# Optimization experiments

Hardware: AMD Instinct MI355X
Metric: run time of the kernel (lower is better)

Reference implementation:

```python
import jax, jax.numpy as jnp
import numpy as np

N, T, D, H = 100000, 16, 8, 40
HP1 = H + 1
ALPHA_DP = 1.0
KAPPA0 = 1000.0   # priorGaussianVarKappa
NU0 = 100.0       # priorWishartNu
PSI0_SCALE = 500.0  # priorWishartPsi = 500*I


def setup_inputs() -> dict:
    key = jax.random.key(0)
    ks = jax.random.split(key, 6)
    return {
        "BetaGamma1": jnp.ones((1, T), jnp.float32),
        "Phi": jax.random.uniform(ks[0], (N, T), jnp.float32),
        "inputData": jax.random.normal(ks[1], (N, D), jnp.float32),
        "outputData": jax.random.normal(ks[2], (N, 1), jnp.float32),
        "weightELM": jax.random.uniform(ks[3], (D, H), jnp.float32) * 2.0 - 1.0,
        "biasELM": jax.random.normal(ks[4], (H, 1), jnp.float32),
        "epsilonA": jnp.ones((1, T), jnp.float32),
        "epsilonB": jnp.ones((1, T), jnp.float32),
        "zetaA": 1e-4 * jnp.ones((1, T), jnp.float32),
        "zetaB": jnp.ones((1, T), jnp.float32),
    }


def reference(BetaGamma1, Phi, inputData, outputData, weightELM, biasELM,
              epsilonA, epsilonB, zetaA, zetaB):
    f32 = jnp.float32
    mu0 = jnp.zeros((D, 1), f32)                      # priorGaussianMeanMu
    Psi0 = PSI0_SCALE * jnp.eye(D, dtype=f32)         # priorWishartPsi

    sumPhi = jnp.sum(Phi, axis=0, keepdims=True)      # [1,T]

    # stick-breaking Beta params. Torch builds a flipped [T,N,T] tril mask;
    # mathematically BetaGamma2[t] = alpha + sum_{j>t} sum_n Phi[n,j]
    BetaGamma1_new = jnp.ones_like(BetaGamma1) + sumPhi
    col = sumPhi[0]                                   # [T]
    rev_incl = jnp.cumsum(col[::-1])[::-1]            # sum_{j>=t}
    BetaGamma2 = (ALPHA_DP + (rev_incl - col))[None, :]

    # Gaussian-Wishart natural-parameter updates.
    # Torch loops over clusters doing [N,D,D] bmm outer products; this is
    # S[:,:,t] = sum_n Phi[n,t] x_n x_n^T
    S = jnp.einsum('nt,ni,nj->ijt', Phi, inputData, inputData)  # [D,D,T]
    t11 = -0.5 * (Psi0 + KAPPA0 * mu0 @ mu0.T)[:, :, None] - 0.5 * S
    t12 = KAPPA0 * mu0 + inputData.T @ Phi            # [D,T]
    t21 = -0.5 * sumPhi - 0.5 * (NU0 + D + 2)         # [1,T]
    kappa = KAPPA0 + sumPhi                           # [1,T]
    mu = t12 / kappa                                  # [D,T]
    nu = -2.0 * t21 - 2.0 - float(D)                  # [1,T]
    psi = -2.0 * t11 - kappa[0][None, None, :] * jnp.einsum('it,jt->ijt', mu, mu)

    # ELM feature map + augmented design matrix X = [sigmoid(x W + b), 1]
    hmap = jax.nn.sigmoid(inputData @ weightELM + biasELM.T)   # [N,H]
    X = jnp.concatenate([hmap, jnp.ones((inputData.shape[0], 1), f32)], axis=1)  # [N,HP1]

    epsExp = (epsilonA / epsilonB)[0]                 # [T]
    zetaExp = (zetaA / zetaB)[0]                      # [T]

    # A[t] = X^T diag(Phi[:,t]) X   (torch: per-cluster bmm with diag_embed)
    A = jnp.einsum('nt,ni,nj->tij', Phi, X, X)        # [T,HP1,HP1]
    WS = jnp.linalg.inv(epsExp[:, None, None] * A
                        + zetaExp[:, None, None] * jnp.eye(HP1, dtype=f32))
    # b[t] = X^T diag(Phi[:,t]) y
    b = jnp.einsum('ni,nt->ti', X * outputData, Phi)  # [T,HP1]
    WMv = zetaExp[:, None] * jnp.einsum('tij,tj->ti', WS, b)   # [T,HP1]
    WM = WMv[:, :, None]                              # [T,HP1,1]

    # prior Zeta/Epsilon alias the variational initial values in __init__
    zetaA_new = zetaA + (H + 1) * 0.5
    zetaB_new = zetaB + 0.5 * (jnp.sum(WMv * WMv, axis=1)
                               + jnp.trace(WS, axis1=-2, axis2=-1))[None, :]
    epsA_new = epsilonA + 0.5 * sumPhi

    pred = jnp.einsum('ni,ti->tn', X, WMv)            # [T,N]
    err = outputData.T - pred                          # [T,N]
    t1 = jnp.einsum('tn,nt->t', err * err, Phi)[None, :]
    t2 = jnp.einsum('tij,tji->t', A, WS)[None, :]
    epsB_new = epsilonB + 0.5 * (t1 + t2)

    return (BetaGamma1_new, BetaGamma2, mu, kappa, nu, psi,
            WM, WS, zetaA_new, zetaB_new, epsA_new, epsB_new)
```

## Files before the change

kernel.cpp:

```cpp
#include <hip/hip_runtime.h>

#define Nn 100000
#define Tt 16
#define Dd 8
#define Hh 40
#define HP1 41

#define CSZ 53248
#define XEF_OFF  0
#define XEH_OFF  (XEF_OFF + 64 * Nn)
#define XEL_OFF  (XEH_OFF + 32 * Nn)
#define PHIT_OFF (XEL_OFF + 32 * Nn)
#define PART_OFF (PHIT_OFF + 16 * Nn)
#define P_OFF    (PART_OFF + 8 * CSZ)

#define OFF_BG1   0
#define OFF_BG2   16
#define OFF_MU    32
#define OFF_KAPPA 160
#define OFF_NU    176
#define OFF_PSI   192
#define OFF_WM    1216
#define OFF_WS    1872
#define OFF_ZA    28768
#define OFF_ZB    28784
#define OFF_EA    28800
#define OFF_EB    28816

typedef _Float16 f16x8 __attribute__((ext_vector_type(8)));
typedef float f32x4 __attribute__((ext_vector_type(4)));
typedef unsigned int u32x4 __attribute__((ext_vector_type(4)));

#define AIDX(i, t, j) ((((i) * 16 + (t)) * 64) + (j))

__global__ __launch_bounds__(256)
void elm_expand(const float* __restrict__ Phi, const float* __restrict__ Xd,
                const float* __restrict__ Yd, const float* __restrict__ W,
                const float* __restrict__ bb, float* __restrict__ XeF32,
                unsigned short* __restrict__ XeHi, unsigned short* __restrict__ XeLo,
                float* __restrict__ PhiT)
{
  __shared__ float sW[Dd * Hh];
  __shared__ float sb[Hh];
  __shared__ float xs[64][9];
  __shared__ float ys[64];
  __shared__ float hrow[64][41];
  __shared__ float pt[16][68];
  int tid = threadIdx.x;
  int n0 = blockIdx.x * 64;

  for (int i = tid; i < Dd * Hh; i += 256) sW[i] = W[i];
  if (tid < Hh) sb[tid] = bb[tid];
  if (tid < 128) {
    int nl = tid >> 1, h4 = (tid & 1) * 4;
    int gn = n0 + nl;
    float4 v = (gn < Nn) ? *(const float4*)(Xd + (size_t)gn * 8 + h4)
                         : make_float4(0.f, 0.f, 0.f, 0.f);
    xs[nl][h4 + 0] = v.x; xs[nl][h4 + 1] = v.y;
    xs[nl][h4 + 2] = v.z; xs[nl][h4 + 3] = v.w;
  }
  if (tid < 64) { int gn = n0 + tid; ys[tid] = (gn < Nn) ? Yd[gn] : 0.f; }
  {
    int nl = tid >> 2, q = tid & 3;
    int gn = n0 + nl;
    float4 v = (gn < Nn) ? *(const float4*)(Phi + (size_t)gn * 16 + q * 4)
                         : make_float4(0.f, 0.f, 0.f, 0.f);
    pt[q * 4 + 0][nl] = v.x; pt[q * 4 + 1][nl] = v.y;
    pt[q * 4 + 2][nl] = v.z; pt[q * 4 + 3][nl] = v.w;
  }
  __syncthreads();
  {
    int nl = tid >> 2, hq = (tid & 3) * 10;
    for (int hh = 0; hh < 10; ++hh) {
      int h = hq + hh;
      float z = sb[h];
#pragma unroll
      for (int d = 0; d < 8; ++d) z = fmaf(xs[nl][d], sW[d * Hh + h], z);
      hrow[nl][h] = 1.f / (1.f + __expf(-z));
    }
  }
  __syncthreads();
  {
    int t = tid & 15, nq = tid >> 4;
    int gn = n0 + nq * 4;
    if (gn < Nn) {
      float4 v = make_float4(pt[t][nq * 4 + 0], pt[t][nq * 4 + 1],
                             pt[t][nq * 4 + 2], pt[t][nq * 4 + 3]);
      *(float4*)(PhiT + (size_t)t * Nn + gn) = v;
    }
  }
  {
    int cidx = tid >> 2, seg = tid & 3;
    int nl0 = seg * 16;
    float vv[16];
#pragma unroll
    for (int j = 0; j < 16; ++j) {
      int n = nl0 + j;
      float v;
      if (cidx < Hh) v = hrow[n][cidx];
      else if (cidx == 40) v = 1.f;
      else if (cidx < 49) v = xs[n][cidx - 41];
      else if (cidx == 49) v = ys[n];
      else v = 0.f;
      vv[j] = v;
    }
#pragma unroll
    for (int q2 = 0; q2 < 4; ++q2) {
      int gn = n0 + nl0 + q2 * 4;
      if (gn < Nn)
        *(float4*)(XeF32 + (size_t)cidx * Nn + gn) =
            make_float4(vv[q2 * 4], vv[q2 * 4 + 1], vv[q2 * 4 + 2], vv[q2 * 4 + 3]);
    }
    unsigned short hs[16], ls[16];
#pragma unroll
    for (int j = 0; j < 16; ++j) {
      _Float16 h = (_Float16)vv[j];
      float r = vv[j] - (float)h;
      _Float16 lo = (_Float16)r;
      hs[j] = __builtin_bit_cast(unsigned short, h);
      ls[j] = __builtin_bit_cast(unsigned short, lo);
    }
#pragma unroll
    for (int q2 = 0; q2 < 2; ++q2) {
      int gn = n0 + nl0 + q2 * 8;
      if (gn < Nn) {
        uint4 uh, ul;
        uh.x = hs[q2*8+0] | ((unsigned)hs[q2*8+1] << 16);
        uh.y = hs[q2*8+2] | ((unsigned)hs[q2*8+3] << 16);
        uh.z = hs[q2*8+4] | ((unsigned)hs[q2*8+5] << 16);
        uh.w = hs[q2*8+6] | ((unsigned)hs[q2*8+7] << 16);
        ul.x = ls[q2*8+0] | ((unsigned)ls[q2*8+1] << 16);
        ul.y = ls[q2*8+2] | ((unsigned)ls[q2*8+3] << 16);
        ul.z = ls[q2*8+4] | ((unsigned)ls[q2*8+5] << 16);
        ul.w = ls[q2*8+6] | ((unsigned)ls[q2*8+7] << 16);
        *(uint4*)(XeHi + (size_t)cidx * Nn + gn) = uh;
        *(uint4*)(XeLo + (size_t)cidx * Nn + gn) = ul;
      }
    }
  }
}

__device__ __forceinline__ void gload16(const void* g, void* l) {
  __builtin_amdgcn_global_load_lds(
      (const __attribute__((address_space(1))) unsigned int*)g,
      (__attribute__((address_space(3))) unsigned int*)l, 16, 0, 0);
}

__global__ __launch_bounds__(256, 2)
void gram_mfma(const float* __restrict__ PhiT, const float* __restrict__ XeF32,
               const unsigned short* __restrict__ XeHi,
               const unsigned short* __restrict__ XeLo,
               float* __restrict__ P, int CH, int KCe)
{
  __shared__ __align__(16) char smem[2][12288];

  int id = blockIdx.x;
  int low3 = id & 7, rest = id >> 3;
  int bM = rest & 3, chigh = rest >> 2;
  int c = chigh * 8 + low3;
  if (c >= KCe) return;

  int tid = threadIdx.x;
  int l = tid & 63, w = tid >> 6;
  int l15 = l & 15, lg = l >> 4;
  int n0 = c * CH;
  int rem = Nn - n0; if (rem > CH) rem = CH;
  int nsteps = rem >> 5;
  int i0 = bM * 13;

  const char* gp[3];
  int gstep[3];
  int ldoff[3];
  {
    int idq = w * 3;
#pragma unroll
    for (int q = 0; q < 3; ++q) {
      int sid = idq + q;
      ldoff[q] = sid * 1024;
      if (sid < 8) {
        int qq = sid & 3;
        int row = 16 * qq + (l >> 2);
        int g = (l & 3) ^ ((l >> 3) & 3);
        const unsigned short* basep = (sid < 4) ? XeHi : XeLo;
        gp[q] = (const char*)(basep + (size_t)row * Nn + n0 + 8 * g);
        gstep[q] = 64;
      } else if (sid < 10) {
        int qq = sid - 8;
        int row = 8 * qq + (l >> 3);
        gp[q] = (const char*)(XeF32 + (size_t)(i0 + row) * Nn + n0 + 4 * (l & 7));
        gstep[q] = 128;
      } else {
        int qq = sid - 10;
        int row = 8 * qq + (l >> 3);
        int g = (l & 7) ^ (l >> 3);
        gp[q] = (const char*)(PhiT + (size_t)row * Nn + n0 + 4 * g);
        gstep[q] = 128;
      }
    }
  }

#define STAGE(buf) do {                          \
    char* db = &smem[buf][0];                    \
    gload16(gp[0], db + ldoff[0]); gp[0] += gstep[0]; \
    gload16(gp[1], db + ldoff[1]); gp[1] += gstep[1]; \
    gload16(gp[2], db + ldoff[2]); gp[2] += gstep[2]; \
  } while (0)

  int sB = (l15 >> 1) & 3;
  int off_b[4];
#pragma unroll
  for (int nt = 0; nt < 4; ++nt)
    off_b[nt] = (l15 + 16 * nt) * 64 + 16 * (lg ^ sB);
  int off_a[4];
#pragma unroll
  for (int mi = 0; mi < 4; ++mi)
    off_a[mi] = 8192 + (4 * w + mi) * 128 + 32 * lg;
  int off_p0 = 10240 + l15 * 128 + 16 * ((2 * lg) ^ (l15 & 7));
  int off_p1 = 10240 + l15 * 128 + 16 * ((2 * lg + 1) ^ (l15 & 7));

  f32x4 acc[4][4];
#pragma unroll
  for (int mi = 0; mi < 4; ++mi)
#pragma unroll
    for (int nt = 0; nt < 4; ++nt) acc[mi][nt] = (f32x4){0.f, 0.f, 0.f, 0.f};

  STAGE(0);
  __syncthreads();

  for (int s = 0; s < nsteps; ++s) {
    int cur = s & 1;
    if (s + 1 < nsteps) STAGE(cur ^ 1);

    const char* base = &smem[cur][0];
    f32x4 p0 = *(const f32x4*)(base + off_p0);
    f32x4 p1 = *(const f32x4*)(base + off_p1);
    f16x8 bh[4], bl[4];
#pragma unroll
    for (int nt = 0; nt < 4; ++nt) {
      bh[nt] = *(const f16x8*)(base + off_b[nt]);
      bl[nt] = *(const f16x8*)(base + 4096 + off_b[nt]);
    }
#pragma unroll
    for (int mi = 0; mi < 4; ++mi) {
      f32x4 x0 = *(const f32x4*)(base + off_a[mi]);
      f32x4 x1 = *(const f32x4*)(base + off_a[mi] + 16);
      float v0 = p0[0] * x0[0], v1 = p0[1] * x0[1];
      float v2 = p0[2] * x0[2], v3 = p0[3] * x0[3];
      float v4 = p1[0] * x1[0], v5 = p1[1] * x1[1];
      float v6 = p1[2] * x1[2], v7 = p1[3] * x1[3];
      auto h0 = __builtin_amdgcn_cvt_pkrtz(v0, v1);
      auto h1 = __builtin_amdgcn_cvt_pkrtz(v2, v3);
      auto h2 = __builtin_amdgcn_cvt_pkrtz(v4, v5);
      auto h3 = __builtin_amdgcn_cvt_pkrtz(v6, v7);
      float r0 = v0 - (float)h0[0], r1 = v1 - (float)h0[1];
      float r2 = v2 - (float)h1[0], r3 = v3 - (float)h1[1];
      float r4 = v4 - (float)h2[0], r5 = v5 - (float)h2[1];
      float r6 = v6 - (float)h3[0], r7 = v7 - (float)h3[1];
      auto e0 = __builtin_amdgcn_cvt_pkrtz(r0, r1);
      auto e1 = __builtin_amdgcn_cvt_pkrtz(r2, r3);
      auto e2 = __builtin_amdgcn_cvt_pkrtz(r4, r5);
      auto e3 = __builtin_amdgcn_cvt_pkrtz(r6, r7);
      u32x4 uh = {__builtin_bit_cast(unsigned int, h0), __builtin_bit_cast(unsigned int, h1),
                  __builtin_bit_cast(unsigned int, h2), __builtin_bit_cast(unsigned int, h3)};
      u32x4 ul = {__builtin_bit_cast(unsigned int, e0), __builtin_bit_cast(unsigned int, e1),
                  __builtin_bit_cast(unsigned int, e2), __builtin_bit_cast(unsigned int, e3)};
      f16x8 ah = __builtin_bit_cast(f16x8, uh);
      f16x8 al = __builtin_bit_cast(f16x8, ul);
#pragma unroll
      for (int nt = 0; nt < 4; ++nt) {
        acc[mi][nt] = __builtin_amdgcn_mfma_f32_16x16x32_f16(ah, bh[nt], acc[mi][nt], 0, 0, 0);
        acc[mi][nt] = __builtin_amdgcn_mfma_f32_16x16x32_f16(ah, bl[nt], acc[mi][nt], 0, 0, 0);
        acc[mi][nt] = __builtin_amdgcn_mfma_f32_16x16x32_f16(al, bh[nt], acc[mi][nt], 0, 0, 0);
      }
    }
    __syncthreads();
  }
#undef STAGE

  float* Pc = P + (size_t)c * CSZ;
#pragma unroll
  for (int mi = 0; mi < 4; ++mi) {
    int mloc = 4 * w + mi;
    if (mloc < 13) {
      int i = i0 + mloc;
#pragma unroll
      for (int nt = 0; nt < 4; ++nt) {
        int j = nt * 16 + l15;
#pragma unroll
        for (int r = 0; r < 4; ++r)
          Pc[(i * 16 + lg * 4 + r) * 64 + j] = acc[mi][nt][r];
      }
    }
  }
}

__global__ __launch_bounds__(256)
void reduce_a(const float4* __restrict__ P4, int nchunks, float4* __restrict__ part4)
{
  int g = blockIdx.y;
  int idx = blockIdx.x * 256 + threadIdx.x;
  int per = (nchunks + 7) / 8;
  int c0 = g * per, c1 = c0 + per; if (c1 > nchunks) c1 = nchunks;
  float4 s = make_float4(0.f, 0.f, 0.f, 0.f);
  for (int cc = c0; cc < c1; ++cc) {
    float4 v = P4[(size_t)cc * (CSZ / 4) + idx];
    s.x += v.x; s.y += v.y; s.z += v.z; s.w += v.w;
  }
  part4[(size_t)g * (CSZ / 4) + idx] = s;
}

__device__ __forceinline__ float accv(const float* __restrict__ part, int idx) {
  float s = 0.f;
#pragma unroll
  for (int g = 0; g < 8; ++g) s += part[g * CSZ + idx];
  return s;
}

__global__ __launch_bounds__(256)
void finalize_kernel(const float* __restrict__ part, const float* __restrict__ epsA,
                     const float* __restrict__ epsB, const float* __restrict__ zetA,
                     const float* __restrict__ zetB, float* __restrict__ out)
{
  int t = blockIdx.x;
  int tid = threadIdx.x;
  __shared__ float G[HP1][84];
  __shared__ float As[HP1][HP1 + 1];
  __shared__ float bs[HP1];
  __shared__ float colk[HP1];
  __shared__ float red[256];
  __shared__ float wmv[HP1];
  __shared__ float rowv[4][HP1 + 1];
  __shared__ float mus[Dd];

  float epsExp = epsA[t] / epsB[t];
  float zetaExp = zetA[t] / zetB[t];

  for (int idx = tid; idx < HP1 * HP1; idx += 256) {
    int i = idx / HP1, j = idx % HP1;
    float a = accv(part, AIDX(i, t, j));
    As[i][j] = a;
    G[i][j] = epsExp * a + (i == j ? zetaExp : 0.f);
    G[i][41 + j] = (i == j) ? 1.f : 0.f;
  }
  for (int idx = tid; idx < HP1; idx += 256) {
    G[idx][82] = 0.f; G[idx][83] = 0.f;
    bs[idx] = accv(part, AIDX(idx, t, 49));
  }
  __syncthreads();

  int c = tid % HP1;
  int ig = tid / HP1;
  int irow0 = ig * 7;

  for (int k = 0; k < HP1; ++k) {
    float pivinv = 1.f / G[k][k];
    if (tid >= 1 && tid <= HP1) G[k][k + tid] *= pivinv;
    if (tid < HP1) colk[tid] = (tid == k) ? 0.f : G[tid][k];
    __syncthreads();
    if (ig < 6) {
      int j = k + 1 + c;
      float pk = G[k][j];
#pragma unroll
      for (int r = 0; r < 7; ++r) {
        int i = irow0 + r;
        if (i < HP1 && i != k) G[i][j] = fmaf(-colk[i], pk, G[i][j]);
      }
    }
    __syncthreads();
  }

  for (int idx = tid; idx < HP1 * HP1; idx += 256) {
    int i = idx / HP1, j = idx % HP1;
    out[OFF_WS + (t * HP1 + i) * HP1 + j] = G[i][41 + j];
  }
  if (tid < HP1) {
    float s = 0.f;
    for (int j = 0; j < HP1; ++j) s += G[tid][41 + j] * bs[j];
    float w = zetaExp * s;
    wmv[tid] = w;
    out[OFF_WM + t * HP1 + tid] = w;
  }
  __syncthreads();
  float lt2 = 0.f;
  for (int idx = tid; idx < HP1 * HP1; idx += 256) {
    int i = idx / HP1, j = idx % HP1;
    lt2 += As[i][j] * G[i][41 + j];
  }
  red[tid] = lt2; __syncthreads();
  for (int s = 128; s > 0; s >>= 1) {
    if (tid < s) red[tid] += red[tid + s];
    __syncthreads();
  }
  float t2v = red[0];
  if (tid < HP1) {
    float w = wmv[tid];
    float aw = 0.f;
    for (int j = 0; j < HP1; ++j) aw += As[tid][j] * wmv[j];
    rowv[0][tid] = w * bs[tid];
    rowv[1][tid] = w * w;
    rowv[2][tid] = G[tid][41 + tid];
    rowv[3][tid] = w * aw;
  }
  __syncthreads();

  float sp = accv(part, AIDX(40, t, 40));
  float kap = 1000.f + sp;
  float syy = accv(part, AIDX(49, t, 49));

  if (tid == 0) {
    float wb = 0.f, wn = 0.f, trc = 0.f, quad = 0.f;
    for (int i = 0; i < HP1; ++i) {
      wb += rowv[0][i]; wn += rowv[1][i]; trc += rowv[2][i]; quad += rowv[3][i];
    }
    float t1 = syy - 2.f * wb + quad;
    out[OFF_BG1 + t] = 1.f + sp;
    float rest = 0.f;
    for (int u = t + 1; u < Tt; ++u) rest += accv(part, AIDX(40, u, 40));
    out[OFF_BG2 + t] = 1.f + rest;
    out[OFF_KAPPA + t] = kap;
    out[OFF_NU + t] = sp + 100.f;
    out[OFF_ZA + t] = zetA[t] + 0.5f * (float)HP1;
    out[OFF_ZB + t] = zetB[t] + 0.5f * (wn + trc);
    out[OFF_EA + t] = epsA[t] + 0.5f * sp;
    out[OFF_EB + t] = epsB[t] + 0.5f * (t1 + t2v);
  }
  if (tid < Dd) {
    float m = accv(part, AIDX(40, t, 41 + tid)) / kap;
    mus[tid] = m;
    out[OFF_MU + tid * Tt + t] = m;
  }
  __syncthreads();
  if (tid < Dd * Dd) {
    int i = tid / Dd, j = tid % Dd;
    float S = accv(part, AIDX(41 + i, t, 41 + j));
    float v = (i == j ? 500.f : 0.f) + S - kap * mus[i] * mus[j];
    out[OFF_PSI + (i * Dd + j) * Tt + t] = v;
  }
}

extern "C" void kernel_launch(void* const* d_in, const int* in_sizes, int n_in,
                              void* d_out, int out_size, void* d_ws, size_t ws_size,
                              hipStream_t stream) {
  const float* Phi = (const float*)d_in[1];
  const float* Xd  = (const float*)d_in[2];
  const float* Yd  = (const float*)d_in[3];
  const float* W   = (const float*)d_in[4];
  const float* bb  = (const float*)d_in[5];
  const float* eA  = (const float*)d_in[6];
  const float* eB  = (const float*)d_in[7];
  const float* zA  = (const float*)d_in[8];
  const float* zB  = (const float*)d_in[9];
  float* out = (float*)d_out;
  float* ws  = (float*)d_ws;

  float* XeF32 = ws + XEF_OFF;
  unsigned short* XeHi = (unsigned short*)(ws + XEH_OFF);
  unsigned short* XeLo = (unsigned short*)(ws + XEL_OFF);
  float* PhiT = ws + PHIT_OFF;
  float* part = ws + PART_OFF;
  float* P    = ws + P_OFF;

  long maxChunks = ((long)(ws_size / 4) - (long)P_OFF) / CSZ;
  if (maxChunks < 1) maxChunks = 1;
  long sp = (3125 + maxChunks - 1) / maxChunks;
  if (sp < 13) sp = 13;
  int CH = (int)(32 * sp);
  int KCe = (Nn + CH - 1) / CH;
  int grid1 = 32 * ((KCe + 7) / 8);

  hipLaunchKernelGGL(elm_expand, dim3((Nn + 63) / 64), dim3(256), 0, stream,
                     Phi, Xd, Yd, W, bb, XeF32, XeHi, XeLo, PhiT);
  hipLaunchKernelGGL(gram_mfma, dim3(grid1), dim3(256), 0, stream,
                     PhiT, XeF32, XeHi, XeLo, P, CH, KCe);
  hipLaunchKernelGGL(reduce_a, dim3(52, 8), dim3(256), 0, stream,
                     (const float4*)P, KCe, (float4*)part);
  hipLaunchKernelGGL(finalize_kernel, dim3(Tt), dim3(256), 0, stream,
                     part, eA, eB, zA, zB, out);
}
```

Baseline: 177.6 us.

## Drop fp32 Xe copy and give each gram block all 52 rows

Removes the fp32 expanded-feature array and rebuilds the A-side values from the hi+lo fp16 split already staged in shared memory. The gram kernel now runs one 512-thread block per N-chunk that covers all 52 output rows (7 or 6 per wave), replacing four row-group blocks that each re-loaded the same B tiles. This cuts global writes in the expand kernel and redundant global/LDS traffic in the gram kernel. The cost is more accumulator registers per wave and a different chunk-count heuristic, with a cap of 256 chunks.

```diff
diff --git a/kernel.cpp b/kernel.cpp
--- a/kernel.cpp
+++ b/kernel.cpp
@@ -7,8 +7,7 @@
 #define HP1 41
 
 #define CSZ 53248
-#define XEF_OFF  0
-#define XEH_OFF  (XEF_OFF + 64 * Nn)
+#define XEH_OFF  0
 #define XEL_OFF  (XEH_OFF + 32 * Nn)
 #define PHIT_OFF (XEL_OFF + 32 * Nn)
 #define PART_OFF (PHIT_OFF + 16 * Nn)
@@ -36,7 +35,7 @@
 __global__ __launch_bounds__(256)
 void elm_expand(const float* __restrict__ Phi, const float* __restrict__ Xd,
                 const float* __restrict__ Yd, const float* __restrict__ W,
-                const float* __restrict__ bb, float* __restrict__ XeF32,
+                const float* __restrict__ bb,
                 unsigned short* __restrict__ XeHi, unsigned short* __restrict__ XeLo,
                 float* __restrict__ PhiT)
 {
@@ -103,13 +102,6 @@
       else if (cidx == 49) v = ys[n];
       else v = 0.f;
       vv[j] = v;
-    }
-#pragma unroll
-    for (int q2 = 0; q2 < 4; ++q2) {
-      int gn = n0 + nl0 + q2 * 4;
-      if (gn < Nn)
-        *(float4*)(XeF32 + (size_t)cidx * Nn + gn) =
-            make_float4(vv[q2 * 4], vv[q2 * 4 + 1], vv[q2 * 4 + 2], vv[q2 * 4 + 3]);
     }
     unsigned short hs[16], ls[16];
 #pragma unroll
@@ -146,81 +138,61 @@
       (__attribute__((address_space(3))) unsigned int*)l, 16, 0, 0);
 }
 
-__global__ __launch_bounds__(256, 2)
-void gram_mfma(const float* __restrict__ PhiT, const float* __restrict__ XeF32,
+__global__ __launch_bounds__(512, 2)
+void gram_mfma(const float* __restrict__ PhiT,
                const unsigned short* __restrict__ XeHi,
                const unsigned short* __restrict__ XeLo,
-               float* __restrict__ P, int CH, int KCe)
+               float* __restrict__ P, int CH)
 {
-  __shared__ __align__(16) char smem[2][12288];
-
-  int id = blockIdx.x;
-  int low3 = id & 7, rest = id >> 3;
-  int bM = rest & 3, chigh = rest >> 2;
-  int c = chigh * 8 + low3;
-  if (c >= KCe) return;
+  __shared__ __align__(16) char smem[2][10240];
 
   int tid = threadIdx.x;
+  int c = blockIdx.x;
   int l = tid & 63, w = tid >> 6;
   int l15 = l & 15, lg = l >> 4;
   int n0 = c * CH;
   int rem = Nn - n0; if (rem > CH) rem = CH;
   int nsteps = rem >> 5;
-  int i0 = bM * 13;
-
-  const char* gp[3];
-  int gstep[3];
-  int ldoff[3];
+
+  int MT  = (w < 4) ? 7 : 6;
+  int i0w = (w < 4) ? 7 * w : 28 + 6 * (w - 4);
+
+  const char* g0; const char* g1 = nullptr;
+  int ld0 = tid * 16, ld1 = (512 + tid) * 16;
   {
-    int idq = w * 3;
-#pragma unroll
-    for (int q = 0; q < 3; ++q) {
-      int sid = idq + q;
-      ldoff[q] = sid * 1024;
-      if (sid < 8) {
-        int qq = sid & 3;
-        int row = 16 * qq + (l >> 2);
-        int g = (l & 3) ^ ((l >> 3) & 3);
-        const unsigned short* basep = (sid < 4) ? XeHi : XeLo;
-        gp[q] = (const char*)(basep + (size_t)row * Nn + n0 + 8 * g);
-        gstep[q] = 64;
-      } else if (sid < 10) {
-        int qq = sid - 8;
-        int row = 8 * qq + (l >> 3);
-        gp[q] = (const char*)(XeF32 + (size_t)(i0 + row) * Nn + n0 + 4 * (l & 7));
-        gstep[q] = 128;
-      } else {
-        int qq = sid - 10;
-        int row = 8 * qq + (l >> 3);
-        int g = (l & 7) ^ (l >> 3);
-        gp[q] = (const char*)(PhiT + (size_t)row * Nn + n0 + 4 * g);
-        gstep[q] = 128;
-      }
-    }
-  }
-
-#define STAGE(buf) do {                          \
-    char* db = &smem[buf][0];                    \
-    gload16(gp[0], db + ldoff[0]); gp[0] += gstep[0]; \
-    gload16(gp[1], db + ldoff[1]); gp[1] += gstep[1]; \
-    gload16(gp[2], db + ldoff[2]); gp[2] += gstep[2]; \
+    int r = (tid & 255) >> 2, s = tid & 3;
+    const unsigned short* bp = (tid < 256) ? XeHi : XeLo;
+    g0 = (const char*)(bp + (size_t)r * Nn + n0 + 8 * (s ^ (r & 3)));
+    if (tid < 128) {
+      int t = tid >> 3, s2 = tid & 7;
+      g1 = (const char*)(PhiT + (size_t)t * Nn + n0 + 4 * (s2 ^ (t & 7)));
+    }
+  }
+
+#define STAGE(buf) do {                              \
+    char* db = &smem[buf][0];                        \
+    gload16(g0, db + ld0); g0 += 64;                 \
+    if (tid < 128) { gload16(g1, db + ld1); g1 += 128; } \
   } while (0)
 
-  int sB = (l15 >> 1) & 3;
   int off_b[4];
 #pragma unroll
-  for (int nt = 0; nt < 4; ++nt)
-    off_b[nt] = (l15 + 16 * nt) * 64 + 16 * (lg ^ sB);
-  int off_a[4];
-#pragma unroll
-  for (int mi = 0; mi < 4; ++mi)
-    off_a[mi] = 8192 + (4 * w + mi) * 128 + 32 * lg;
-  int off_p0 = 10240 + l15 * 128 + 16 * ((2 * lg) ^ (l15 & 7));
-  int off_p1 = 10240 + l15 * 128 + 16 * ((2 * lg + 1) ^ (l15 & 7));
-
-  f32x4 acc[4][4];
-#pragma unroll
-  for (int mi = 0; mi < 4; ++mi)
+  for (int nt = 0; nt < 4; ++nt) {
+    int j = l15 + 16 * nt;
+    off_b[nt] = j * 64 + 16 * (lg ^ (j & 3));
+  }
+  int off_p0 = 8192 + l15 * 128 + 16 * ((2 * lg) ^ (l15 & 7));
+  int off_p1 = 8192 + l15 * 128 + 16 * ((2 * lg + 1) ^ (l15 & 7));
+  int off_a[7];
+#pragma unroll
+  for (int mi = 0; mi < 7; ++mi) {
+    int i = i0w + mi;
+    off_a[mi] = i * 64 + 16 * (lg ^ (i & 3));
+  }
+
+  f32x4 acc[7][4];
+#pragma unroll
+  for (int mi = 0; mi < 7; ++mi)
 #pragma unroll
     for (int nt = 0; nt < 4; ++nt) acc[mi][nt] = (f32x4){0.f, 0.f, 0.f, 0.f};
 
@@ -234,6 +206,8 @@
     const char* base = &smem[cur][0];
     f32x4 p0 = *(const f32x4*)(base + off_p0);
     f32x4 p1 = *(const f32x4*)(base + off_p1);
+    float ph[8] = {p0[0], p0[1], p0[2], p0[3], p1[0], p1[1], p1[2], p1[3]};
+
     f16x8 bh[4], bl[4];
 #pragma unroll
     for (int nt = 0; nt < 4; ++nt) {
@@ -241,13 +215,18 @@
       bl[nt] = *(const f16x8*)(base + 4096 + off_b[nt]);
     }
 #pragma unroll
-    for (int mi = 0; mi < 4; ++mi) {
-      f32x4 x0 = *(const f32x4*)(base + off_a[mi]);
-      f32x4 x1 = *(const f32x4*)(base + off_a[mi] + 16);
-      float v0 = p0[0] * x0[0], v1 = p0[1] * x0[1];
-      float v2 = p0[2] * x0[2], v3 = p0[3] * x0[3];
-      float v4 = p1[0] * x1[0], v5 = p1[1] * x1[1];
-      float v6 = p1[2] * x1[2], v7 = p1[3] * x1[3];
+    for (int mi = 0; mi < 7; ++mi) {
+      if (mi >= MT) break;
+      f16x8 xh = *(const f16x8*)(base + off_a[mi]);
+      f16x8 xl = *(const f16x8*)(base + 4096 + off_a[mi]);
+      float v0 = ph[0] * ((float)xh[0] + (float)xl[0]);
+      float v1 = ph[1] * ((float)xh[1] + (float)xl[1]);
+      float v2 = ph[2] * ((float)xh[2] + (float)xl[2]);
+      float v3 = ph[3] * ((float)xh[3] + (float)xl[3]);
+      float v4 = ph[4] * ((float)xh[4] + (float)xl[4]);
+      float v5 = ph[5] * ((float)xh[5] + (float)xl[5]);
+      float v6 = ph[6] * ((float)xh[6] + (float)xl[6]);
+      float v7 = ph[7] * ((float)xh[7] + (float)xl[7]);
       auto h0 = __builtin_amdgcn_cvt_pkrtz(v0, v1);
       auto h1 = __builtin_amdgcn_cvt_pkrtz(v2, v3);
       auto h2 = __builtin_amdgcn_cvt_pkrtz(v4, v5);
@@ -279,17 +258,15 @@
 
   float* Pc = P + (size_t)c * CSZ;
 #pragma unroll
-  for (int mi = 0; mi < 4; ++mi) {
-    int mloc = 4 * w + mi;
-    if (mloc < 13) {
-      int i = i0 + mloc;
-#pragma unroll
-      for (int nt = 0; nt < 4; ++nt) {
-        int j = nt * 16 + l15;
-#pragma unroll
-        for (int r = 0; r < 4; ++r)
-          Pc[(i * 16 + lg * 4 + r) * 64 + j] = acc[mi][nt][r];
-      }
+  for (int mi = 0; mi < 7; ++mi) {
+    if (mi >= MT) break;
+    int i = i0w + mi;
+#pragma unroll
+    for (int nt = 0; nt < 4; ++nt) {
+      int j = nt * 16 + l15;
+#pragma unroll
+      for (int r = 0; r < 4; ++r)
+        Pc[(i * 16 + lg * 4 + r) * 64 + j] = acc[mi][nt][r];
     }
   }
 }
@@ -453,7 +430,6 @@
   float* out = (float*)d_out;
   float* ws  = (float*)d_ws;
 
-  float* XeF32 = ws + XEF_OFF;
   unsigned short* XeHi = (unsigned short*)(ws + XEH_OFF);
   unsigned short* XeLo = (unsigned short*)(ws + XEL_OFF);
   float* PhiT = ws + PHIT_OFF;
@@ -462,16 +438,15 @@
 
   long maxChunks = ((long)(ws_size / 4) - (long)P_OFF) / CSZ;
   if (maxChunks < 1) maxChunks = 1;
-  long sp = (3125 + maxChunks - 1) / maxChunks;
-  if (sp < 13) sp = 13;
+  long cap = maxChunks < 256 ? maxChunks : 256;
+  long sp = (3125 + cap - 1) / cap;
   int CH = (int)(32 * sp);
   int KCe = (Nn + CH - 1) / CH;
-  int grid1 = 32 * ((KCe + 7) / 8);
 
   hipLaunchKernelGGL(elm_expand, dim3((Nn + 63) / 64), dim3(256), 0, stream,
-                     Phi, Xd, Yd, W, bb, XeF32, XeHi, XeLo, PhiT);
-  hipLaunchKernelGGL(gram_mfma, dim3(grid1), dim3(256), 0, stream,
-                     PhiT, XeF32, XeHi, XeLo, P, CH, KCe);
+                     Phi, Xd, Yd, W, bb, XeHi, XeLo, PhiT);
+  hipLaunchKernelGGL(gram_mfma, dim3(KCe), dim3(512), 0, stream,
+                     PhiT, XeHi, XeLo, P, CH);
   hipLaunchKernelGGL(reduce_a, dim3(52, 8), dim3(256), 0, stream,
                      (const float4*)P, KCe, (float4*)part);
   hipLaunchKernelGGL(finalize_kernel, dim3(Tt), dim3(256), 0, stream,
```

After: 170.6 us. 1.04x faster.
